# Kernel tuning notes

Measured on AMD Instinct MI355X. Metric: run time of the kernel, lower is better.

## Reference

```python
import jax, jax.numpy as jnp
import numpy as np

B, L, H, E = 8, 4096, 8, 64
NEIGH = 128          # neigh_size: local window length (entries per row of band mask)
SPLITS = 32          # number of Q blocks
L1 = L // SPLITS     # rows per block = 128 (neigh_size <= L/splits holds with equality)


def setup_inputs() -> dict:
    key = jax.random.key(0)
    kq, kk, kv = jax.random.split(key, 3)
    return {
        "queries": jax.random.normal(kq, (B, L, H, E), jnp.float32),
        "keys":    jax.random.normal(kk, (B, L, H, E), jnp.float32),
        "values":  jax.random.normal(kv, (B, L, H, E), jnp.float32),
    }


def reference(queries, keys, values):
    scale = 1.0 / np.sqrt(E)
    # Global key index of each entry in a KV block: block j covers [j*l1 - neigh, j*l1 + l1)
    kv_idx = (jnp.arange(SPLITS)[:, None] * L1
              + jnp.arange(L1 + NEIGH)[None, :] - NEIGH)      # [splits, l1+neigh]
    kv_gather = jnp.clip(kv_idx, 0, L - 1)                    # out-of-range entries get masked

    Qb = queries.reshape(B, SPLITS, L1, H, E)                 # [B, j, l, H, E]
    Kb = keys[:, kv_gather]                                   # [B, j, m, H, E]
    Vb = values[:, kv_gather]                                 # [B, j, m, H, E]

    scores = jnp.einsum('bjlhe,bjmhe->bhjlm', Qb, Kb) * scale # [B, H, splits, l1, l1+neigh]

    # Band: key global index k satisfies q - neigh < k <= q  <=>  l < m <= l + neigh
    l_idx = jnp.arange(L1)[:, None]
    m_idx = jnp.arange(L1 + NEIGH)[None, :]
    band = (m_idx > l_idx) & (m_idx <= l_idx + NEIGH)         # [l1, l1+neigh]
    valid = band[None, :, :] & (kv_idx[:, None, :] >= 0)      # [splits, l1, l1+neigh]

    scores = jnp.where(valid[None, None], scores, jnp.float32(-1e9))
    attn = jax.nn.softmax(scores, axis=-1)
    out = jnp.einsum('bhjlm,bjmhe->bjlhe', attn, Vb)          # [B, splits, l1, H, E]
    return out.reshape(B, L, H, E)
```

## Files before the change

### kernel.cpp

```cpp
#include <hip/hip_runtime.h>

#define B_ 8
#define L_ 4096
#define H_ 8
#define E_ 64
#define NEIGH_ 128
#define SPLITS_ 32
#define BQ 128
#define WIN 256
#define KPAD 72

typedef float f32x4 __attribute__((ext_vector_type(4)));
typedef __bf16 bf16x8 __attribute__((ext_vector_type(8)));
typedef unsigned short u16x4 __attribute__((ext_vector_type(4)));
typedef unsigned short u16x8 __attribute__((ext_vector_type(8)));
typedef unsigned int u32;

__device__ inline unsigned short f2bf(float f) {
  unsigned int u = __float_as_uint(f);
  u += 0x7fff + ((u >> 16) & 1);
  return (unsigned short)(u >> 16);
}
__device__ inline u32 pack2(float a, float b) {
  return (u32)f2bf(a) | ((u32)f2bf(b) << 16);
}

__global__ __launch_bounds__(512, 4) void la_kernel(
    const float* __restrict__ Q, const float* __restrict__ K,
    const float* __restrict__ V, float* __restrict__ out) {
  const int j = blockIdx.x, h = blockIdx.y, b = blockIdx.z;
  const int t = threadIdx.x;

  __shared__ unsigned short Ks[WIN * KPAD];
  __shared__ u32 Vs32[E_ * (WIN / 2)];

  const int q0 = j * BQ;
  const int g0 = q0 - NEIGH_;

  for (int i = 0; i < 8; ++i) {
    int idx = t + i * 512;
    int km = idx >> 4, c4 = idx & 15;
    int g = g0 + km; g = g < 0 ? 0 : g;
    const float4 v = *(const float4*)(K + ((((size_t)b * L_) + g) * H_ + h) * E_ + c4 * 4);
    u16x4 p = { f2bf(v.x), f2bf(v.y), f2bf(v.z), f2bf(v.w) };
    *(u16x4*)&Ks[km * KPAD + c4 * 4] = p;
  }
  for (int i = 0; i < 4; ++i) {
    int idx = t + i * 512;
    int kp = idx >> 4, c4 = idx & 15;
    int k0g = g0 + 2 * kp, k1g = k0g + 1;
    k0g = k0g < 0 ? 0 : k0g; k1g = k1g < 0 ? 0 : k1g;
    const float4 v0 = *(const float4*)(V + ((((size_t)b * L_) + k0g) * H_ + h) * E_ + c4 * 4);
    const float4 v1 = *(const float4*)(V + ((((size_t)b * L_) + k1g) * H_ + h) * E_ + c4 * 4);
    int g = kp >> 2;
    int ko = kp & 3;
    const float a0[4] = {v0.x, v0.y, v0.z, v0.w};
    const float a1[4] = {v1.x, v1.y, v1.z, v1.w};
#pragma unroll
    for (int w = 0; w < 4; ++w) {
      int e = c4 * 4 + w;
      int gs = g ^ (e & 31);
      Vs32[e * 128 + gs * 4 + ko] = pack2(a0[w], a1[w]);
    }
  }

  const int wv = t >> 6, lane = t & 63;
  const int l15 = lane & 15, quad = lane >> 4;
  const int r0 = wv * 16;
  const int lq = r0 + l15;

  bf16x8 qfrag[2];
  {
    const float* qrow = Q + ((((size_t)b * L_) + q0 + lq) * H_ + h) * E_;
#pragma unroll
    for (int ks = 0; ks < 2; ++ks) {
      const float4 x = *(const float4*)(qrow + ks * 32 + quad * 8);
      const float4 y = *(const float4*)(qrow + ks * 32 + quad * 8 + 4);
      u16x8 p = { f2bf(x.x), f2bf(x.y), f2bf(x.z), f2bf(x.w),
                  f2bf(y.x), f2bf(y.y), f2bf(y.z), f2bf(y.w) };
      qfrag[ks] = __builtin_bit_cast(bf16x8, p);
    }
  }
  __syncthreads();

  f32x4 S[16];
#pragma unroll
  for (int kt = 0; kt < 16; ++kt) S[kt] = (f32x4){0.f, 0.f, 0.f, 0.f};
#pragma unroll
  for (int ks = 0; ks < 2; ++ks) {
#pragma unroll
    for (int kt = 0; kt < 16; ++kt) {
      bf16x8 a = __builtin_bit_cast(bf16x8,
          *(const u16x8*)&Ks[(kt * 16 + l15) * KPAD + ks * 32 + quad * 8]);
      S[kt] = __builtin_amdgcn_mfma_f32_16x16x32_bf16(a, qfrag[ks], S[kt], 0, 0, 0);
    }
  }

  float m = -1e30f;
#pragma unroll
  for (int kt = 0; kt < 16; ++kt) {
#pragma unroll
    for (int r = 0; r < 4; ++r) {
      int key = kt * 16 + quad * 4 + r;
      float s = S[kt][r] * 0.125f;
      bool valid = (key > lq) & (key <= lq + NEIGH_) & (g0 + key >= 0);
      s = valid ? s : -1e30f;
      S[kt][r] = s;
      m = fmaxf(m, s);
    }
  }
  m = fmaxf(m, __shfl_xor(m, 16));
  m = fmaxf(m, __shfl_xor(m, 32));

  float lsum = 0.f;
  u32 pk[16][2];
#pragma unroll
  for (int kt = 0; kt < 16; ++kt) {
    float p0 = __expf(S[kt][0] - m);
    float p1 = __expf(S[kt][1] - m);
    float p2 = __expf(S[kt][2] - m);
    float p3 = __expf(S[kt][3] - m);
    lsum += (p0 + p1) + (p2 + p3);
    pk[kt][0] = pack2(p0, p1);
    pk[kt][1] = pack2(p2, p3);
  }
  lsum += __shfl_xor(lsum, 16);
  lsum += __shfl_xor(lsum, 32);
  const float inv = 1.0f / lsum;

  f32x4 O[4];
#pragma unroll
  for (int et = 0; et < 4; ++et) O[et] = (f32x4){0.f, 0.f, 0.f, 0.f};
  const int srcBase = 16 * ((quad & 1) * 2) + l15;
  const bool hiTile = (quad >> 1) != 0;
#pragma unroll
  for (int ks = 0; ks < 8; ++ks) {
    u32 a32[4];
#pragma unroll
    for (int k = 0; k < 4; ++k) {
      int src = srcBase + 16 * (k >> 1);
      u32 u0 = (u32)__shfl((int)pk[2 * ks][k & 1], src);
      u32 u1 = (u32)__shfl((int)pk[2 * ks + 1][k & 1], src);
      a32[k] = hiTile ? u1 : u0;
    }
    bf16x8 afrag = __builtin_bit_cast(bf16x8,
        (u32 __attribute__((ext_vector_type(4)))){a32[0], a32[1], a32[2], a32[3]});
#pragma unroll
    for (int et = 0; et < 4; ++et) {
      int e = et * 16 + l15;
      int gs = (ks * 4 + quad) ^ (e & 31);
      bf16x8 bfrag = __builtin_bit_cast(bf16x8,
          *(const u16x8*)((const unsigned short*)Vs32 + e * 256 + gs * 8));
      O[et] = __builtin_amdgcn_mfma_f32_16x16x32_bf16(afrag, bfrag, O[et], 0, 0, 0);
    }
  }

  float invq[4];
#pragma unroll
  for (int r = 0; r < 4; ++r) invq[r] = __shfl(inv, quad * 4 + r);
#pragma unroll
  for (int et = 0; et < 4; ++et)
#pragma unroll
    for (int r = 0; r < 4; ++r) {
      int row = r0 + quad * 4 + r;
      out[((((size_t)b * L_) + q0 + row) * H_ + h) * E_ + et * 16 + l15] = O[et][r] * invq[r];
    }
}

extern "C" void kernel_launch(void* const* d_in, const int* in_sizes, int n_in,
                              void* d_out, int out_size, void* d_ws, size_t ws_size,
                              hipStream_t stream) {
  const float* q = (const float*)d_in[0];
  const float* k = (const float*)d_in[1];
  const float* v = (const float*)d_in[2];
  float* o = (float*)d_out;
  dim3 grid(SPLITS_, H_, B_);
  la_kernel<<<grid, 512, 0, stream>>>(q, k, v, o);
}
```

Before: 221.9 us.

## Process four query blocks per workgroup with double-buffered K/V halves and prefetch

Each workgroup now handles four consecutive 128-row query blocks and keeps the K/V window as two 128-row halves in a ring of shared-memory buffers. The overlapping half is reused from the previous block, so each K/V row is loaded and converted to bf16 once instead of twice. Loads for the next half are issued into registers before the QK and PV math, which hides global latency. In exchange the grid has a quarter as many workgroups (512), register pressure rises from the prefetch registers, and two barriers are added per block. The bf16 conversion now uses the native cast and the V swizzle pattern is changed.

Result: slower. 267.1 us (+20.4%).

```diff
diff --git a/kernel.cpp b/kernel.cpp
--- a/kernel.cpp
+++ b/kernel.cpp
@@ -5,10 +5,10 @@
 #define H_ 8
 #define E_ 64
 #define NEIGH_ 128
-#define SPLITS_ 32
+#define NJ 4
 #define BQ 128
-#define WIN 256
-#define KPAD 72
+#define KROW 72
+#define HE 512
 
 typedef float f32x4 __attribute__((ext_vector_type(4)));
 typedef __bf16 bf16x8 __attribute__((ext_vector_type(8)));
@@ -17,154 +17,225 @@
 typedef unsigned int u32;
 
 __device__ inline unsigned short f2bf(float f) {
-  unsigned int u = __float_as_uint(f);
-  u += 0x7fff + ((u >> 16) & 1);
-  return (unsigned short)(u >> 16);
+  return __builtin_bit_cast(unsigned short, (__bf16)f);
 }
 __device__ inline u32 pack2(float a, float b) {
   return (u32)f2bf(a) | ((u32)f2bf(b) << 16);
+}
+__device__ inline int vsig(int e) {
+  return ((e & 15) ^ ((e >> 2) & 7)) & 7;
 }
 
 __global__ __launch_bounds__(512, 4) void la_kernel(
     const float* __restrict__ Q, const float* __restrict__ K,
     const float* __restrict__ V, float* __restrict__ out) {
-  const int j = blockIdx.x, h = blockIdx.y, b = blockIdx.z;
+  const int jg = blockIdx.x, h = blockIdx.y, b = blockIdx.z;
   const int t = threadIdx.x;
 
-  __shared__ unsigned short Ks[WIN * KPAD];
-  __shared__ u32 Vs32[E_ * (WIN / 2)];
-
-  const int q0 = j * BQ;
-  const int g0 = q0 - NEIGH_;
-
-  for (int i = 0; i < 8; ++i) {
-    int idx = t + i * 512;
-    int km = idx >> 4, c4 = idx & 15;
-    int g = g0 + km; g = g < 0 ? 0 : g;
-    const float4 v = *(const float4*)(K + ((((size_t)b * L_) + g) * H_ + h) * E_ + c4 * 4);
-    u16x4 p = { f2bf(v.x), f2bf(v.y), f2bf(v.z), f2bf(v.w) };
-    *(u16x4*)&Ks[km * KPAD + c4 * 4] = p;
-  }
-  for (int i = 0; i < 4; ++i) {
-    int idx = t + i * 512;
-    int kp = idx >> 4, c4 = idx & 15;
-    int k0g = g0 + 2 * kp, k1g = k0g + 1;
-    k0g = k0g < 0 ? 0 : k0g; k1g = k1g < 0 ? 0 : k1g;
-    const float4 v0 = *(const float4*)(V + ((((size_t)b * L_) + k0g) * H_ + h) * E_ + c4 * 4);
-    const float4 v1 = *(const float4*)(V + ((((size_t)b * L_) + k1g) * H_ + h) * E_ + c4 * 4);
-    int g = kp >> 2;
-    int ko = kp & 3;
-    const float a0[4] = {v0.x, v0.y, v0.z, v0.w};
-    const float a1[4] = {v1.x, v1.y, v1.z, v1.w};
-#pragma unroll
-    for (int w = 0; w < 4; ++w) {
-      int e = c4 * 4 + w;
-      int gs = g ^ (e & 31);
-      Vs32[e * 128 + gs * 4 + ko] = pack2(a0[w], a1[w]);
-    }
-  }
-
+  __shared__ unsigned short Ks[2][BQ * KROW];
+  __shared__ u32 Vs[2][E_ * 64];
+
+  const size_t bh = (size_t)b * (L_ * HE) + h * E_;
+  const float* Qp = Q + bh;
+  const float* Kp = K + bh;
+  const float* Vp = V + bh;
+  float* Op = out + bh;
+
+  const int base = jg * (NJ * BQ);
   const int wv = t >> 6, lane = t & 63;
   const int l15 = lane & 15, quad = lane >> 4;
   const int r0 = wv * 16;
   const int lq = r0 + l15;
 
-  bf16x8 qfrag[2];
-  {
-    const float* qrow = Q + ((((size_t)b * L_) + q0 + lq) * H_ + h) * E_;
-#pragma unroll
-    for (int ks = 0; ks < 2; ++ks) {
-      const float4 x = *(const float4*)(qrow + ks * 32 + quad * 8);
-      const float4 y = *(const float4*)(qrow + ks * 32 + quad * 8 + 4);
-      u16x8 p = { f2bf(x.x), f2bf(x.y), f2bf(x.z), f2bf(x.w),
-                  f2bf(y.x), f2bf(y.y), f2bf(y.z), f2bf(y.w) };
-      qfrag[ks] = __builtin_bit_cast(bf16x8, p);
+  for (int half = 0; half < 2; ++half) {
+    const int buf = 1 - half;
+    const int gs = base - NEIGH_ + half * NEIGH_;
+    for (int i = 0; i < 4; ++i) {
+      int idx = t + i * 512;
+      int row = idx >> 4, c4 = idx & 15;
+      int g = gs + row; g = g < 0 ? 0 : g;
+      const float4 v = *(const float4*)(Kp + (size_t)g * HE + c4 * 4);
+      *(u16x4*)&Ks[buf][row * KROW + c4 * 4] =
+          (u16x4){f2bf(v.x), f2bf(v.y), f2bf(v.z), f2bf(v.w)};
+    }
+    for (int i = 0; i < 2; ++i) {
+      int idx = t + i * 512;
+      int kp = idx >> 4, c4 = idx & 15;
+      int ga = gs + 2 * kp, gb = ga + 1;
+      ga = ga < 0 ? 0 : ga; gb = gb < 0 ? 0 : gb;
+      const float4 va = *(const float4*)(Vp + (size_t)ga * HE + c4 * 4);
+      const float4 vb = *(const float4*)(Vp + (size_t)gb * HE + c4 * 4);
+      const float fa[4] = {va.x, va.y, va.z, va.w};
+      const float fb[4] = {vb.x, vb.y, vb.z, vb.w};
+      int g4 = kp >> 2, ko = kp & 3;
+#pragma unroll
+      for (int w = 0; w < 4; ++w) {
+        int e = c4 * 4 + w;
+        Vs[buf][e * 64 + (((g4 ^ vsig(e)) << 2) | ko)] = pack2(fa[w], fb[w]);
+      }
     }
   }
   __syncthreads();
 
-  f32x4 S[16];
-#pragma unroll
-  for (int kt = 0; kt < 16; ++kt) S[kt] = (f32x4){0.f, 0.f, 0.f, 0.f};
-#pragma unroll
-  for (int ks = 0; ks < 2; ++ks) {
+  for (int j = 0; j < NJ; ++j) {
+    const int q0 = base + j * BQ;
+    const int g0 = q0 - NEIGH_;
+    const int lob = (j + 1) & 1, hib = j & 1;
+    const bool pf = (j + 1 < NJ);
+    const int gn = q0 + BQ;
+
+    bf16x8 qfrag[2];
+    {
+      const float* qrow = Qp + (size_t)(q0 + lq) * HE;
+#pragma unroll
+      for (int ks = 0; ks < 2; ++ks) {
+        const float4 x = *(const float4*)(qrow + ks * 32 + quad * 8);
+        const float4 y = *(const float4*)(qrow + ks * 32 + quad * 8 + 4);
+        qfrag[ks] = __builtin_bit_cast(bf16x8,
+            (u16x8){f2bf(x.x), f2bf(x.y), f2bf(x.z), f2bf(x.w),
+                    f2bf(y.x), f2bf(y.y), f2bf(y.z), f2bf(y.w)});
+      }
+    }
+
+    float4 nK[4];
+    if (pf) {
+#pragma unroll
+      for (int i = 0; i < 4; ++i) {
+        int idx = t + i * 512;
+        int row = idx >> 4, c4 = idx & 15;
+        nK[i] = *(const float4*)(Kp + (size_t)(gn + row) * HE + c4 * 4);
+      }
+    }
+
+    f32x4 S[16];
+#pragma unroll
+    for (int kt = 0; kt < 16; ++kt) S[kt] = (f32x4){0.f, 0.f, 0.f, 0.f};
+#pragma unroll
+    for (int ks = 0; ks < 2; ++ks) {
+#pragma unroll
+      for (int kt = 0; kt < 16; ++kt) {
+        const unsigned short* kb = (kt < 8)
+            ? &Ks[lob][(kt * 16 + l15) * KROW]
+            : &Ks[hib][((kt - 8) * 16 + l15) * KROW];
+        bf16x8 a = __builtin_bit_cast(bf16x8, *(const u16x8*)(kb + ks * 32 + quad * 8));
+        S[kt] = __builtin_amdgcn_mfma_f32_16x16x32_bf16(a, qfrag[ks], S[kt], 0, 0, 0);
+      }
+    }
+
+    float m = -1e30f;
 #pragma unroll
     for (int kt = 0; kt < 16; ++kt) {
-      bf16x8 a = __builtin_bit_cast(bf16x8,
-          *(const u16x8*)&Ks[(kt * 16 + l15) * KPAD + ks * 32 + quad * 8]);
-      S[kt] = __builtin_amdgcn_mfma_f32_16x16x32_bf16(a, qfrag[ks], S[kt], 0, 0, 0);
-    }
-  }
-
-  float m = -1e30f;
-#pragma unroll
-  for (int kt = 0; kt < 16; ++kt) {
-#pragma unroll
-    for (int r = 0; r < 4; ++r) {
-      int key = kt * 16 + quad * 4 + r;
-      float s = S[kt][r] * 0.125f;
-      bool valid = (key > lq) & (key <= lq + NEIGH_) & (g0 + key >= 0);
-      s = valid ? s : -1e30f;
-      S[kt][r] = s;
-      m = fmaxf(m, s);
-    }
-  }
-  m = fmaxf(m, __shfl_xor(m, 16));
-  m = fmaxf(m, __shfl_xor(m, 32));
-
-  float lsum = 0.f;
-  u32 pk[16][2];
-#pragma unroll
-  for (int kt = 0; kt < 16; ++kt) {
-    float p0 = __expf(S[kt][0] - m);
-    float p1 = __expf(S[kt][1] - m);
-    float p2 = __expf(S[kt][2] - m);
-    float p3 = __expf(S[kt][3] - m);
-    lsum += (p0 + p1) + (p2 + p3);
-    pk[kt][0] = pack2(p0, p1);
-    pk[kt][1] = pack2(p2, p3);
-  }
-  lsum += __shfl_xor(lsum, 16);
-  lsum += __shfl_xor(lsum, 32);
-  const float inv = 1.0f / lsum;
-
-  f32x4 O[4];
-#pragma unroll
-  for (int et = 0; et < 4; ++et) O[et] = (f32x4){0.f, 0.f, 0.f, 0.f};
-  const int srcBase = 16 * ((quad & 1) * 2) + l15;
-  const bool hiTile = (quad >> 1) != 0;
-#pragma unroll
-  for (int ks = 0; ks < 8; ++ks) {
-    u32 a32[4];
-#pragma unroll
-    for (int k = 0; k < 4; ++k) {
-      int src = srcBase + 16 * (k >> 1);
-      u32 u0 = (u32)__shfl((int)pk[2 * ks][k & 1], src);
-      u32 u1 = (u32)__shfl((int)pk[2 * ks + 1][k & 1], src);
-      a32[k] = hiTile ? u1 : u0;
-    }
-    bf16x8 afrag = __builtin_bit_cast(bf16x8,
-        (u32 __attribute__((ext_vector_type(4)))){a32[0], a32[1], a32[2], a32[3]});
+#pragma unroll
+      for (int r = 0; r < 4; ++r) {
+        int key = kt * 16 + quad * 4 + r;
+        float s = S[kt][r] * 0.125f;
+        bool valid = (key > lq) & (key <= lq + NEIGH_) & (g0 + key >= 0);
+        s = valid ? s : -1e30f;
+        S[kt][r] = s;
+        m = fmaxf(m, s);
+      }
+    }
+    m = fmaxf(m, __shfl_xor(m, 16));
+    m = fmaxf(m, __shfl_xor(m, 32));
+
+    float lsum = 0.f;
+    u32 pk[16][2];
+#pragma unroll
+    for (int kt = 0; kt < 16; ++kt) {
+      float p0 = __expf(S[kt][0] - m);
+      float p1 = __expf(S[kt][1] - m);
+      float p2 = __expf(S[kt][2] - m);
+      float p3 = __expf(S[kt][3] - m);
+      lsum += (p0 + p1) + (p2 + p3);
+      pk[kt][0] = pack2(p0, p1);
+      pk[kt][1] = pack2(p2, p3);
+    }
+    lsum += __shfl_xor(lsum, 16);
+    lsum += __shfl_xor(lsum, 32);
+    const float inv = 1.0f / lsum;
+
+    float4 nV[4];
+    if (pf) {
+#pragma unroll
+      for (int i = 0; i < 2; ++i) {
+        int idx = t + i * 512;
+        int kp = idx >> 4, c4 = idx & 15;
+        nV[2 * i]     = *(const float4*)(Vp + (size_t)(gn + 2 * kp) * HE + c4 * 4);
+        nV[2 * i + 1] = *(const float4*)(Vp + (size_t)(gn + 2 * kp + 1) * HE + c4 * 4);
+      }
+    }
+
+    f32x4 O[4];
+#pragma unroll
+    for (int et = 0; et < 4; ++et) O[et] = (f32x4){0.f, 0.f, 0.f, 0.f};
+    int vbase[4], sig[4];
 #pragma unroll
     for (int et = 0; et < 4; ++et) {
       int e = et * 16 + l15;
-      int gs = (ks * 4 + quad) ^ (e & 31);
-      bf16x8 bfrag = __builtin_bit_cast(bf16x8,
-          *(const u16x8*)((const unsigned short*)Vs32 + e * 256 + gs * 8));
-      O[et] = __builtin_amdgcn_mfma_f32_16x16x32_bf16(afrag, bfrag, O[et], 0, 0, 0);
+      vbase[et] = e * 64;
+      sig[et] = vsig(e);
+    }
+    const int srcBase = 16 * ((quad & 1) * 2) + l15;
+    const bool hiTile = (quad >> 1) != 0;
+#pragma unroll
+    for (int ks = 0; ks < 8; ++ks) {
+      u32 a32[4];
+#pragma unroll
+      for (int k = 0; k < 4; ++k) {
+        int src = srcBase + 16 * (k >> 1);
+        u32 u0 = (u32)__shfl((int)pk[2 * ks][k & 1], src);
+        u32 u1 = (u32)__shfl((int)pk[2 * ks + 1][k & 1], src);
+        a32[k] = hiTile ? u1 : u0;
+      }
+      bf16x8 afrag = __builtin_bit_cast(bf16x8,
+          (u32 __attribute__((ext_vector_type(4)))){a32[0], a32[1], a32[2], a32[3]});
+      const u32* vb = (ks < 4) ? &Vs[lob][0] : &Vs[hib][0];
+      const int ks4 = ks & 3;
+#pragma unroll
+      for (int et = 0; et < 4; ++et) {
+        int word = vbase[et] + ((((ks4 * 4 + quad) ^ sig[et])) << 2);
+        bf16x8 bfrag = __builtin_bit_cast(bf16x8, *(const u16x8*)((const unsigned short*)(vb + word)));
+        O[et] = __builtin_amdgcn_mfma_f32_16x16x32_bf16(afrag, bfrag, O[et], 0, 0, 0);
+      }
+    }
+
+    float invq[4];
+#pragma unroll
+    for (int r = 0; r < 4; ++r) invq[r] = __shfl(inv, quad * 4 + r);
+#pragma unroll
+    for (int et = 0; et < 4; ++et)
+#pragma unroll
+      for (int r = 0; r < 4; ++r) {
+        int row = r0 + quad * 4 + r;
+        Op[(size_t)(q0 + row) * HE + et * 16 + l15] = O[et][r] * invq[r];
+      }
+
+    if (pf) {
+      __syncthreads();
+#pragma unroll
+      for (int i = 0; i < 4; ++i) {
+        int idx = t + i * 512;
+        int row = idx >> 4, c4 = idx & 15;
+        *(u16x4*)&Ks[lob][row * KROW + c4 * 4] =
+            (u16x4){f2bf(nK[i].x), f2bf(nK[i].y), f2bf(nK[i].z), f2bf(nK[i].w)};
+      }
+#pragma unroll
+      for (int i = 0; i < 2; ++i) {
+        int idx = t + i * 512;
+        int kp = idx >> 4, c4 = idx & 15;
+        const float4 va = nV[2 * i], vb2 = nV[2 * i + 1];
+        const float fa[4] = {va.x, va.y, va.z, va.w};
+        const float fb[4] = {vb2.x, vb2.y, vb2.z, vb2.w};
+        int g4 = kp >> 2, ko = kp & 3;
+#pragma unroll
+        for (int w = 0; w < 4; ++w) {
+          int e = c4 * 4 + w;
+          Vs[lob][e * 64 + (((g4 ^ vsig(e)) << 2) | ko)] = pack2(fa[w], fb[w]);
+        }
+      }
+      __syncthreads();
     }
   }
-
-  float invq[4];
-#pragma unroll
-  for (int r = 0; r < 4; ++r) invq[r] = __shfl(inv, quad * 4 + r);
-#pragma unroll
-  for (int et = 0; et < 4; ++et)
-#pragma unroll
-    for (int r = 0; r < 4; ++r) {
-      int row = r0 + quad * 4 + r;
-      out[((((size_t)b * L_) + q0 + row) * H_ + h) * E_ + et * 16 + l15] = O[et][r] * invq[r];
-    }
 }
 
 extern "C" void kernel_launch(void* const* d_in, const int* in_sizes, int n_in,
@@ -174,6 +245,6 @@
   const float* k = (const float*)d_in[1];
   const float* v = (const float*)d_in[2];
   float* o = (float*)d_out;
-  dim3 grid(SPLITS_, H_, B_);
+  dim3 grid(L_ / (NJ * BQ), H_, B_);
   la_kernel<<<grid, 512, 0, stream>>>(q, k, v, o);
 }
```
